# Kernel optimization log

Hardware: AMD Instinct MI355X
Metric: run time of the kernel (lower is better)

The kernel has to match this reference:

```python
import jax, jax.numpy as jnp
import numpy as np

EPS_RMS = 1e-6
EPS_Q = 1e-5


def _weight_quant(w):
    # BitNet b1.58-style ternary weight quantization with mean-abs scale
    scale = 1.0 / jnp.clip(jnp.mean(jnp.abs(w)), EPS_Q)
    wq = jnp.clip(jnp.round(w * scale), -1.0, 1.0) / scale
    return w + jax.lax.stop_gradient(wq - w)  # STE


def _activation_quant(x):
    # per-token 8-bit absmax quantization
    scale = 127.0 / jnp.clip(jnp.max(jnp.abs(x), axis=-1, keepdims=True), EPS_Q)
    xq = jnp.clip(jnp.round(x * scale), -128.0, 127.0) / scale
    return x + jax.lax.stop_gradient(xq - x)  # STE


def _rmsnorm(x, weight):
    inv = jax.lax.rsqrt(jnp.mean(x * x, axis=-1, keepdims=True) + EPS_RMS)
    return x * inv * weight


def setup_inputs() -> dict:
    key = jax.random.key(0)
    k1, k2, k3 = jax.random.split(key, 3)
    B, S, D, CD = 8, 4096, 1024, 1024
    x = jax.random.normal(k1, (B, S, D), dtype=jnp.float32)
    c = jax.random.normal(k2, (B, CD), dtype=jnp.float32)
    # NOTE: the module zero-inits proj; we use small random weights so the
    # quantized conditioning path is numerically exercised.
    w_proj = jax.random.normal(k3, (2 * D, CD), dtype=jnp.float32) * 0.02
    b_proj = jnp.zeros((2 * D,), dtype=jnp.float32)
    rms_weight = jnp.ones((D,), dtype=jnp.float32)
    return {"x": x, "c": c, "w_proj": w_proj, "b_proj": b_proj, "rms_weight": rms_weight}


def reference(x, c, w_proj, b_proj, rms_weight):
    if c.ndim == 2:
        c = c[:, None, :]  # [B, 1, cond_dim]
    # BitLinear: quantized activations x quantized ternary weights
    cq = _activation_quant(c)
    wq = _weight_quant(w_proj)
    emb = jnp.einsum('btc,dc->btd', cq, wq) + b_proj  # [B, 1, 2*dim]
    scale, shift = jnp.split(emb, 2, axis=-1)
    xn = _rmsnorm(x, rms_weight)
    return xn * (1.0 + scale) + shift
```

## Files before the change

### kernel.cpp

```cpp
#include <hip/hip_runtime.h>
#include <math.h>


constexpr int Bn = 8;
constexpr int Sn = 4096;
constexpr int Dn = 1024;
constexpr int TWO_D = 2048;
constexpr int OFF_PART = 0;
constexpr int OFF_CQ   = 4096;
constexpr int OFF_G    = 16384;
constexpr int OFF_SH   = 24576;

using f4 = __attribute__((ext_vector_type(4))) float;

__device__ __forceinline__ float waveReduceSumBcast(float v) {
#pragma unroll
    for (int off = 32; off > 0; off >>= 1) v += __shfl_xor(v, off, 64);
    return v;
}
__device__ __forceinline__ float waveReduceMaxBcast(float v) {
#pragma unroll
    for (int off = 32; off > 0; off >>= 1) v = fmaxf(v, __shfl_xor(v, off, 64));
    return v;
}

__global__ void k_pre(const float* __restrict__ w, const float* __restrict__ c,
                      float* __restrict__ part, float* __restrict__ cq) {
    int tid = threadIdx.x;
    if (blockIdx.x < TWO_D) {
        size_t base = (size_t)blockIdx.x * 1024 + (size_t)tid * 4;
        f4 v = *(const f4*)(w + base);
        float s = fabsf(v.x) + fabsf(v.y) + fabsf(v.z) + fabsf(v.w);
        s = waveReduceSumBcast(s);
        __shared__ float lds[4];
        if ((tid & 63) == 0) lds[tid >> 6] = s;
        __syncthreads();
        if (tid == 0) part[blockIdx.x] = lds[0] + lds[1] + lds[2] + lds[3];
    } else {
        int b = blockIdx.x - TWO_D;
        f4 v = ((const f4*)(c + (size_t)b * Dn))[tid];
        float m = fmaxf(fmaxf(fabsf(v.x), fabsf(v.y)), fmaxf(fabsf(v.z), fabsf(v.w)));
        m = waveReduceMaxBcast(m);
        __shared__ float lm[4];
        if ((tid & 63) == 0) lm[tid >> 6] = m;
        __syncthreads();
        float mx = fmaxf(fmaxf(lm[0], lm[1]), fmaxf(lm[2], lm[3]));
        float scale = 127.0f / fmaxf(mx, 1e-5f);
        float inv = 1.0f / scale;
        f4 q;
        q.x = fminf(fmaxf(rintf(v.x * scale), -128.0f), 127.0f) * inv;
        q.y = fminf(fmaxf(rintf(v.y * scale), -128.0f), 127.0f) * inv;
        q.z = fminf(fmaxf(rintf(v.z * scale), -128.0f), 127.0f) * inv;
        q.w = fminf(fmaxf(rintf(v.w * scale), -128.0f), 127.0f) * inv;
        ((f4*)(cq + (size_t)b * Dn))[tid] = q;
    }
}

__global__ void k_emb(const float* __restrict__ w, const float* __restrict__ bp,
                      const float* __restrict__ cq, const float* __restrict__ part,
                      const float* __restrict__ rw,
                      float* __restrict__ g, float* __restrict__ sh) {
    int tid = threadIdx.x;
    float s = 0.0f;
#pragma unroll
    for (int k = 0; k < 8; ++k) s += part[tid + k * 256];
    s = waveReduceSumBcast(s);
    __shared__ float lds[4];
    if ((tid & 63) == 0) lds[tid >> 6] = s;
    __syncthreads();
    float mw = fmaxf((lds[0] + lds[1] + lds[2] + lds[3]) * (1.0f / 2097152.0f), 1e-5f);
    float sw = 1.0f / mw;

    int lane = tid & 63;
    int d = (blockIdx.x * blockDim.x + tid) >> 6;
    const float* wr = w + (size_t)d * 1024 + (size_t)lane * 16;
    float t[16];
#pragma unroll
    for (int j = 0; j < 16; j += 4) {
        f4 v = *(const f4*)(wr + j);
        t[j + 0] = fminf(fmaxf(rintf(v.x * sw), -1.0f), 1.0f);
        t[j + 1] = fminf(fmaxf(rintf(v.y * sw), -1.0f), 1.0f);
        t[j + 2] = fminf(fmaxf(rintf(v.z * sw), -1.0f), 1.0f);
        t[j + 3] = fminf(fmaxf(rintf(v.w * sw), -1.0f), 1.0f);
    }
    float acc[Bn];
#pragma unroll
    for (int b = 0; b < Bn; ++b) {
        const float* cr = cq + (size_t)b * Dn + (size_t)lane * 16;
        float dot = 0.0f;
#pragma unroll
        for (int j = 0; j < 16; j += 4) {
            f4 u = *(const f4*)(cr + j);
            dot += t[j + 0] * u.x + t[j + 1] * u.y + t[j + 2] * u.z + t[j + 3] * u.w;
        }
        acc[b] = dot;
    }
#pragma unroll
    for (int off = 32; off > 0; off >>= 1) {
#pragma unroll
        for (int b = 0; b < Bn; ++b) acc[b] += __shfl_xor(acc[b], off, 64);
    }
    if (lane == 0) {
        float bias = bp[d];
        if (d < Dn) {
            float rwd = rw[d];
#pragma unroll
            for (int b = 0; b < Bn; ++b)
                g[b * Dn + d] = rwd * (1.0f + (acc[b] * mw + bias));
        } else {
#pragma unroll
            for (int b = 0; b < Bn; ++b)
                sh[b * Dn + (d - Dn)] = acc[b] * mw + bias;
        }
    }
}

__global__ void __launch_bounds__(256) k_main(
        const float* __restrict__ x, const float* __restrict__ g,
        const float* __restrict__ sh, float* __restrict__ out) {
    constexpr int NW = 2048 * 4;
    int tid  = threadIdx.x;
    int lane = tid & 63;
    int row  = blockIdx.x * 4 + (tid >> 6);

    const f4* xr = (const f4*)(x + (size_t)row * Dn);
    f4 v0 = __builtin_nontemporal_load(&xr[lane]);
    f4 v1 = __builtin_nontemporal_load(&xr[lane + 64]);
    f4 v2 = __builtin_nontemporal_load(&xr[lane + 128]);
    f4 v3 = __builtin_nontemporal_load(&xr[lane + 192]);

#pragma unroll
    for (int it = 0; it < 4; ++it) {
        int nrow = row + NW;
        f4 n0, n1, n2, n3;
        if (it < 3) {
            const f4* xn = (const f4*)(x + (size_t)nrow * Dn);
            n0 = __builtin_nontemporal_load(&xn[lane]);
            n1 = __builtin_nontemporal_load(&xn[lane + 64]);
            n2 = __builtin_nontemporal_load(&xn[lane + 128]);
            n3 = __builtin_nontemporal_load(&xn[lane + 192]);
        }
        float ss = v0.x*v0.x + v0.y*v0.y + v0.z*v0.z + v0.w*v0.w
                 + v1.x*v1.x + v1.y*v1.y + v1.z*v1.z + v1.w*v1.w
                 + v2.x*v2.x + v2.y*v2.y + v2.z*v2.z + v2.w*v2.w
                 + v3.x*v3.x + v3.y*v3.y + v3.z*v3.z + v3.w*v3.w;
        ss = waveReduceSumBcast(ss);
        float inv = rsqrtf(ss * (1.0f / 1024.0f) + 1e-6f);

        int b = row >> 12;
        const f4* gv  = (const f4*)(g  + (size_t)b * Dn);
        const f4* s0v = (const f4*)(sh + (size_t)b * Dn);
        f4* ov = (f4*)(out + (size_t)row * Dn);
#pragma unroll
        for (int q = 0; q < 4; ++q) {
            int idx = lane + q * 64;
            f4 v = (q == 0) ? v0 : (q == 1) ? v1 : (q == 2) ? v2 : v3;
            f4 gg = gv[idx];
            f4 s0 = s0v[idx];
            f4 o;
            o.x = v.x * inv * gg.x + s0.x;
            o.y = v.y * inv * gg.y + s0.y;
            o.z = v.z * inv * gg.z + s0.z;
            o.w = v.w * inv * gg.w + s0.w;
            ov[idx] = o;
        }
        if (it < 3) { v0 = n0; v1 = n1; v2 = n2; v3 = n3; row = nrow; }
    }
}

extern "C" void kernel_launch(void* const* d_in, const int* in_sizes, int n_in,
                              void* d_out, int out_size, void* d_ws, size_t ws_size,
                              hipStream_t stream) {
    const float* x  = (const float*)d_in[0];
    const float* c  = (const float*)d_in[1];
    const float* w  = (const float*)d_in[2];
    const float* bp = (const float*)d_in[3];
    const float* rw = (const float*)d_in[4];
    float* out = (float*)d_out;
    float* ws  = (float*)d_ws;

    float* part = ws + OFF_PART;
    float* cq   = ws + OFF_CQ;
    float* g    = ws + OFF_G;
    float* sh   = ws + OFF_SH;

    k_pre <<<TWO_D + Bn, 256, 0, stream>>>(w, c, part, cq);
    k_emb <<<TWO_D / 4, 256, 0, stream>>>(w, bp, cq, part, rw, g, sh);
    k_main<<<TWO_D, 256, 0, stream>>>(x, g, sh, out);
}
```

Measured before the change: 64.66 us.

## Process two rows per wave in one pass instead of a persistent prefetch loop

The main normalization kernel moves from a persistent grid of 2048 blocks, each wave looping over 4 strided rows with software prefetch, to 4096 blocks where each wave handles two adjacent rows in a single pass. It also drops the nontemporal load hints on x. Loading both rows up front and reducing them together gives more memory-level parallelism per wave and reuses the g/shift loads across two rows. In exchange it doubles the block count and loses the explicit load/compute overlap and the cache-bypass hints.

```diff
diff --git a/kernel.cpp b/kernel.cpp
--- a/kernel.cpp
+++ b/kernel.cpp
@@ -3,7 +3,6 @@
 
 
 constexpr int Bn = 8;
-constexpr int Sn = 4096;
 constexpr int Dn = 1024;
 constexpr int TWO_D = 2048;
 constexpr int OFF_PART = 0;
@@ -13,15 +12,18 @@
 
 using f4 = __attribute__((ext_vector_type(4))) float;
 
-__device__ __forceinline__ float waveReduceSumBcast(float v) {
+__device__ __forceinline__ float wsumf(float v) {
 #pragma unroll
-    for (int off = 32; off > 0; off >>= 1) v += __shfl_xor(v, off, 64);
+    for (int o = 32; o > 0; o >>= 1) v += __shfl_xor(v, o, 64);
     return v;
 }
-__device__ __forceinline__ float waveReduceMaxBcast(float v) {
+__device__ __forceinline__ float wmaxf(float v) {
 #pragma unroll
-    for (int off = 32; off > 0; off >>= 1) v = fmaxf(v, __shfl_xor(v, off, 64));
+    for (int o = 32; o > 0; o >>= 1) v = fmaxf(v, __shfl_xor(v, o, 64));
     return v;
+}
+__device__ __forceinline__ float sumsq4(f4 v) {
+    return v.x*v.x + v.y*v.y + v.z*v.z + v.w*v.w;
 }
 
 __global__ void k_pre(const float* __restrict__ w, const float* __restrict__ c,
@@ -31,7 +33,7 @@
         size_t base = (size_t)blockIdx.x * 1024 + (size_t)tid * 4;
         f4 v = *(const f4*)(w + base);
         float s = fabsf(v.x) + fabsf(v.y) + fabsf(v.z) + fabsf(v.w);
-        s = waveReduceSumBcast(s);
+        s = wsumf(s);
         __shared__ float lds[4];
         if ((tid & 63) == 0) lds[tid >> 6] = s;
         __syncthreads();
@@ -40,7 +42,7 @@
         int b = blockIdx.x - TWO_D;
         f4 v = ((const f4*)(c + (size_t)b * Dn))[tid];
         float m = fmaxf(fmaxf(fabsf(v.x), fabsf(v.y)), fmaxf(fabsf(v.z), fabsf(v.w)));
-        m = waveReduceMaxBcast(m);
+        m = wmaxf(m);
         __shared__ float lm[4];
         if ((tid & 63) == 0) lm[tid >> 6] = m;
         __syncthreads();
@@ -64,7 +66,7 @@
     float s = 0.0f;
 #pragma unroll
     for (int k = 0; k < 8; ++k) s += part[tid + k * 256];
-    s = waveReduceSumBcast(s);
+    s = wsumf(s);
     __shared__ float lds[4];
     if ((tid & 63) == 0) lds[tid >> 6] = s;
     __syncthreads();
@@ -96,9 +98,9 @@
         acc[b] = dot;
     }
 #pragma unroll
-    for (int off = 32; off > 0; off >>= 1) {
+    for (int o = 32; o > 0; o >>= 1) {
 #pragma unroll
-        for (int b = 0; b < Bn; ++b) acc[b] += __shfl_xor(acc[b], off, 64);
+        for (int b = 0; b < Bn; ++b) acc[b] += __shfl_xor(acc[b], o, 64);
     }
     if (lane == 0) {
         float bias = bp[d];
@@ -118,53 +120,49 @@
 __global__ void __launch_bounds__(256) k_main(
         const float* __restrict__ x, const float* __restrict__ g,
         const float* __restrict__ sh, float* __restrict__ out) {
-    constexpr int NW = 2048 * 4;
     int tid  = threadIdx.x;
     int lane = tid & 63;
-    int row  = blockIdx.x * 4 + (tid >> 6);
+    int row  = blockIdx.x * 8 + (tid >> 6) * 2;
+    int b    = row >> 12;
 
-    const f4* xr = (const f4*)(x + (size_t)row * Dn);
-    f4 v0 = __builtin_nontemporal_load(&xr[lane]);
-    f4 v1 = __builtin_nontemporal_load(&xr[lane + 64]);
-    f4 v2 = __builtin_nontemporal_load(&xr[lane + 128]);
-    f4 v3 = __builtin_nontemporal_load(&xr[lane + 192]);
+    const f4* xa = (const f4*)(x + (size_t)row * Dn);
+    const f4* xb = xa + 256;
+    f4 a0 = xa[lane], a1 = xa[lane+64], a2 = xa[lane+128], a3 = xa[lane+192];
+    f4 b0 = xb[lane], b1 = xb[lane+64], b2 = xb[lane+128], b3 = xb[lane+192];
+
+    float sa = sumsq4(a0) + sumsq4(a1) + sumsq4(a2) + sumsq4(a3);
+    float sb = sumsq4(b0) + sumsq4(b1) + sumsq4(b2) + sumsq4(b3);
+#pragma unroll
+    for (int o = 32; o > 0; o >>= 1) {
+        sa += __shfl_xor(sa, o, 64);
+        sb += __shfl_xor(sb, o, 64);
+    }
+    float ia = rsqrtf(sa * (1.0f / 1024.0f) + 1e-6f);
+    float ib = rsqrtf(sb * (1.0f / 1024.0f) + 1e-6f);
+
+    const f4* gv = (const f4*)(g  + (size_t)b * Dn);
+    const f4* hv = (const f4*)(sh + (size_t)b * Dn);
+    f4* oa = (f4*)(out + (size_t)row * Dn);
+    f4* ob = oa + 256;
 
 #pragma unroll
-    for (int it = 0; it < 4; ++it) {
-        int nrow = row + NW;
-        f4 n0, n1, n2, n3;
-        if (it < 3) {
-            const f4* xn = (const f4*)(x + (size_t)nrow * Dn);
-            n0 = __builtin_nontemporal_load(&xn[lane]);
-            n1 = __builtin_nontemporal_load(&xn[lane + 64]);
-            n2 = __builtin_nontemporal_load(&xn[lane + 128]);
-            n3 = __builtin_nontemporal_load(&xn[lane + 192]);
-        }
-        float ss = v0.x*v0.x + v0.y*v0.y + v0.z*v0.z + v0.w*v0.w
-                 + v1.x*v1.x + v1.y*v1.y + v1.z*v1.z + v1.w*v1.w
-                 + v2.x*v2.x + v2.y*v2.y + v2.z*v2.z + v2.w*v2.w
-                 + v3.x*v3.x + v3.y*v3.y + v3.z*v3.z + v3.w*v3.w;
-        ss = waveReduceSumBcast(ss);
-        float inv = rsqrtf(ss * (1.0f / 1024.0f) + 1e-6f);
-
-        int b = row >> 12;
-        const f4* gv  = (const f4*)(g  + (size_t)b * Dn);
-        const f4* s0v = (const f4*)(sh + (size_t)b * Dn);
-        f4* ov = (f4*)(out + (size_t)row * Dn);
-#pragma unroll
-        for (int q = 0; q < 4; ++q) {
-            int idx = lane + q * 64;
-            f4 v = (q == 0) ? v0 : (q == 1) ? v1 : (q == 2) ? v2 : v3;
-            f4 gg = gv[idx];
-            f4 s0 = s0v[idx];
-            f4 o;
-            o.x = v.x * inv * gg.x + s0.x;
-            o.y = v.y * inv * gg.y + s0.y;
-            o.z = v.z * inv * gg.z + s0.z;
-            o.w = v.w * inv * gg.w + s0.w;
-            ov[idx] = o;
-        }
-        if (it < 3) { v0 = n0; v1 = n1; v2 = n2; v3 = n3; row = nrow; }
+    for (int q = 0; q < 4; ++q) {
+        int idx = lane + q * 64;
+        f4 va = (q == 0) ? a0 : (q == 1) ? a1 : (q == 2) ? a2 : a3;
+        f4 vb = (q == 0) ? b0 : (q == 1) ? b1 : (q == 2) ? b2 : b3;
+        f4 gg = gv[idx];
+        f4 hh = hv[idx];
+        f4 o;
+        o.x = va.x * ia * gg.x + hh.x;
+        o.y = va.y * ia * gg.y + hh.y;
+        o.z = va.z * ia * gg.z + hh.z;
+        o.w = va.w * ia * gg.w + hh.w;
+        oa[idx] = o;
+        o.x = vb.x * ib * gg.x + hh.x;
+        o.y = vb.y * ib * gg.y + hh.y;
+        o.z = vb.z * ib * gg.z + hh.z;
+        o.w = vb.w * ib * gg.w + hh.w;
+        ob[idx] = o;
     }
 }
 
@@ -186,5 +184,5 @@
 
     k_pre <<<TWO_D + Bn, 256, 0, stream>>>(w, c, part, cq);
     k_emb <<<TWO_D / 4, 256, 0, stream>>>(w, bp, cq, part, rw, g, sh);
-    k_main<<<TWO_D, 256, 0, stream>>>(x, g, sh, out);
+    k_main<<<Bn * 4096 / 8, 256, 0, stream>>>(x, g, sh, out);
 }
```

Measured after the change: 61.18 us. 1.06x faster.
